# Performance work log

Measured on AMD Instinct MI355X. Metric: run time of the kernel, lower is better.

Reference implementation:

```python
import jax, jax.numpy as jnp
import numpy as np

NEG_INF = -1e30
LRELU_SLOPE = 0.2

B, E, IN_DIM, OUT_DIM = 64, 512, 1024, 256


def setup_inputs() -> dict:
    key = jax.random.key(0)
    ks = jax.random.split(key, 6)
    input_state = jax.random.normal(ks[0], (B, E, IN_DIM), dtype=jnp.float32)
    adj = jnp.ones((B, E, E), dtype=jnp.float32)  # only used via ones_like in the original
    node_mask = jax.random.randint(ks[1], (B, E, 1), 0, 2, dtype=jnp.int32)
    W_w = jax.random.normal(ks[2], (OUT_DIM, IN_DIM), dtype=jnp.float32) * (1.0 / np.sqrt(IN_DIM))
    W_b = jax.random.normal(ks[3], (OUT_DIM,), dtype=jnp.float32) * 0.02
    a_w = jax.random.normal(ks[4], (1, 2 * OUT_DIM), dtype=jnp.float32) * (1.0 / np.sqrt(2 * OUT_DIM))
    a_b = jax.random.normal(ks[5], (1,), dtype=jnp.float32) * 0.02
    return {"input_state": input_state, "adj": adj, "node_mask": node_mask,
            "W_w": W_w, "W_b": W_b, "a_w": a_w, "a_b": a_b}


def reference(input_state, adj, node_mask, W_w, W_b, a_w, a_b):
    # h = W(input_state); dropout is identity in eval mode (gnn_drop=0)
    h = jnp.einsum('bei,oi->beo', input_state, W_w) + W_b  # b,E,d
    d = h.shape[-1]
    # a([h_i ; h_j]) decomposes exactly: a_w[:, :d] @ h_i + a_w[:, d:] @ h_j + a_b
    a1, a2 = a_w[:, :d], a_w[:, d:]
    s1 = jnp.einsum('beo,xo->bex', h, a1)  # b,E,1 -> score contribution of source node i
    s2 = jnp.einsum('beo,xo->bex', h, a2)  # b,E,1 -> contribution of target node j
    scores = s1 + jnp.swapaxes(s2, 1, 2) + a_b  # b,E,E, scores[n,i,j] = a([h_i;h_j])
    scores = jnp.where(scores >= 0, scores, LRELU_SLOPE * scores)  # LeakyReLU(0.2)
    # fully-connected adjacency gated by node mask: mask_i * mask_j
    m = node_mask.astype(scores.dtype)  # b,E,1
    pair_mask = m * jnp.swapaxes(m, 1, 2)  # b,E,E
    scores = jnp.where(pair_mask > 0, scores, NEG_INF)
    coefs = jax.nn.softmax(scores, axis=-1)  # b,E,E
    h = h * m  # zero out masked nodes before aggregation
    return jnp.einsum('bij,bjo->bio', coefs, h)
```

## Files before the change

kernel.cpp:

```cpp
#include <hip/hip_runtime.h>
#include <hip/hip_fp16.h>
#include <math.h>

#define NEG_INF_F (-1e30f)
#define LRELU 0.2f

constexpr int Bb = 64, Ee = 512, IND = 1024, OUTD = 256;
constexpr int Mrows = Bb * Ee;

typedef __attribute__((ext_vector_type(8))) _Float16 half8;
typedef __attribute__((ext_vector_type(4))) _Float16 half4;
typedef __attribute__((ext_vector_type(4))) float floatx4;

#define AS1 __attribute__((address_space(1)))
#define AS3 __attribute__((address_space(3)))

__global__ __launch_bounds__(256) void wconv_kernel(
    const float* __restrict__ W, _Float16* __restrict__ Whf)
{
    const int i = (blockIdx.x * 256 + threadIdx.x) * 4;
    const float4 w = *reinterpret_cast<const float4*>(&W[i]);
    half4 hh;
    hh[0] = (_Float16)w.x; hh[1] = (_Float16)w.y;
    hh[2] = (_Float16)w.z; hh[3] = (_Float16)w.w;
    *reinterpret_cast<half4*>(&Whf[i]) = hh;
}

__global__ __launch_bounds__(256) void gemm_h_f16(
    const float* __restrict__ X, const _Float16* __restrict__ Whf,
    const float* __restrict__ Wb, const float* __restrict__ aw,
    const int* __restrict__ mask,
    _Float16* __restrict__ HmTh, _Float16* __restrict__ HmTl,
    float* __restrict__ s1, float* __restrict__ s2)
{
    __shared__ char lds_raw[81920];
    _Float16* As = (_Float16*)lds_raw;
    _Float16* Bs = (_Float16*)(lds_raw + 16384);
    float*    s1p  = (float*)lds_raw;
    float*    s2p  = (float*)(lds_raw + 1024);
    float*    mkfs = (float*)(lds_raw + 2048);
    _Float16* Th   = (_Float16*)(lds_raw + 16384);
    _Float16* Tl   = (_Float16*)(lds_raw + 49152);

    const int t  = threadIdx.x;
    const int w  = t >> 6;
    const int l  = t & 63;
    const int ln = l & 15;
    const int lg = l >> 4;
    const int m0 = blockIdx.x * 64;

    const int mA = t >> 3, pp = t & 7;
    const int aswz = pp ^ (mA & 7);
    const float* __restrict__ xbase = X + (size_t)m0 * IND;

    const int bn_sub = l >> 3;
    const int bkg = (l & 7) ^ (bn_sub & 7);

    floatx4 acc[4][4];
    #pragma unroll
    for (int i = 0; i < 4; ++i)
        #pragma unroll
        for (int j = 0; j < 4; ++j)
            acc[i][j] = (floatx4)0.f;

    auto loadA = [&](int k0, float4 xr[2][2]) {
        #pragma unroll
        for (int i = 0; i < 2; ++i) {
            const float* p = xbase + (size_t)(mA + 32 * i) * IND + k0 + pp * 8;
            xr[i][0] = *reinterpret_cast<const float4*>(p);
            xr[i][1] = *reinterpret_cast<const float4*>(p + 4);
        }
    };
    auto writeA = [&](int buf, float4 xr[2][2]) {
        #pragma unroll
        for (int i = 0; i < 2; ++i) {
            half8 h;
            h[0] = (_Float16)xr[i][0].x; h[1] = (_Float16)xr[i][0].y;
            h[2] = (_Float16)xr[i][0].z; h[3] = (_Float16)xr[i][0].w;
            h[4] = (_Float16)xr[i][1].x; h[5] = (_Float16)xr[i][1].y;
            h[6] = (_Float16)xr[i][1].z; h[7] = (_Float16)xr[i][1].w;
            *reinterpret_cast<half8*>(As + buf * 4096 + (mA + 32 * i) * 64 + aswz * 8) = h;
        }
    };
    auto stageB = [&](int buf, int k0) {
        #pragma unroll
        for (int j = 0; j < 8; ++j) {
            const int n = w * 64 + j * 8 + bn_sub;
            __builtin_amdgcn_global_load_lds(
                (const AS1 unsigned int*)(Whf + (size_t)n * IND + k0 + bkg * 8),
                (AS3 unsigned int*)(Bs + buf * 16384 + w * 4096 + j * 512),
                16, 0, 0);
        }
    };

    {
        float4 xr[2][2];
        loadA(0, xr);
        stageB(0, 0);
        writeA(0, xr);
    }
    __syncthreads();

    #pragma unroll 2
    for (int step = 0; step < 16; ++step) {
        const int buf = step & 1;
        float4 xn[2][2];
        if (step < 15) {
            loadA((step + 1) * 64, xn);
            stageB(buf ^ 1, (step + 1) * 64);
        }

        half8 af[2][4], bf[2][4];
        #pragma unroll
        for (int kk = 0; kk < 2; ++kk) {
            #pragma unroll
            for (int mr = 0; mr < 4; ++mr) {
                const int row = mr * 16 + ln;
                const int ch = (kk * 4 + lg) ^ (ln & 7);
                af[kk][mr] = *reinterpret_cast<const half8*>(As + buf * 4096 + row * 64 + ch * 8);
            }
            #pragma unroll
            for (int nr = 0; nr < 4; ++nr) {
                const int n = w * 64 + nr * 16 + ln;
                const int ch = (kk * 4 + lg) ^ (ln & 7);
                bf[kk][nr] = *reinterpret_cast<const half8*>(Bs + buf * 16384 + n * 64 + ch * 8);
            }
        }
        #pragma unroll
        for (int kk = 0; kk < 2; ++kk)
            #pragma unroll
            for (int mr = 0; mr < 4; ++mr)
                #pragma unroll
                for (int nr = 0; nr < 4; ++nr)
                    acc[mr][nr] = __builtin_amdgcn_mfma_f32_16x16x32_f16(
                        af[kk][mr], bf[kk][nr], acc[mr][nr], 0, 0, 0);

        if (step < 15) writeA(buf ^ 1, xn);
        __syncthreads();
    }

    if (t < 64) mkfs[t] = (float)mask[m0 + t];
    __syncthreads();

    float bias[4], a1c[4], a2c[4];
    #pragma unroll
    for (int nr = 0; nr < 4; ++nr) {
        const int n = w * 64 + nr * 16 + ln;
        bias[nr] = Wb[n];
        a1c[nr]  = aw[n];
        a2c[nr]  = aw[OUTD + n];
    }
    float sv1[4][4], sv2[4][4];
    #pragma unroll
    for (int i = 0; i < 4; ++i)
        #pragma unroll
        for (int r = 0; r < 4; ++r) { sv1[i][r] = 0.f; sv2[i][r] = 0.f; }

    #pragma unroll
    for (int mr = 0; mr < 4; ++mr)
        #pragma unroll
        for (int nr = 0; nr < 4; ++nr) {
            const int n = w * 64 + nr * 16 + ln;
            half4 hh, hl;
            #pragma unroll
            for (int rr = 0; rr < 4; ++rr) {
                const float hb = acc[mr][nr][rr] + bias[nr];
                sv1[mr][rr] += hb * a1c[nr];
                sv2[mr][rr] += hb * a2c[nr];
                const float hm = hb * mkfs[mr * 16 + lg * 4 + rr];
                const _Float16 hhi = (_Float16)hm;
                hh[rr] = hhi;
                hl[rr] = (_Float16)(hm - (float)hhi);
            }
            const int idx = n * 64 + ((mr * 16 + lg * 4) ^ ((n & 7) << 3));
            *reinterpret_cast<half4*>(Th + idx) = hh;
            *reinterpret_cast<half4*>(Tl + idx) = hl;
        }

    #pragma unroll
    for (int mr = 0; mr < 4; ++mr)
        #pragma unroll
        for (int rr = 0; rr < 4; ++rr) {
            float v1 = sv1[mr][rr], v2 = sv2[mr][rr];
            #pragma unroll
            for (int off = 1; off < 16; off <<= 1) {
                v1 += __shfl_xor(v1, off, 64);
                v2 += __shfl_xor(v2, off, 64);
            }
            if (ln == 0) {
                s1p[w * 64 + mr * 16 + lg * 4 + rr] = v1;
                s2p[w * 64 + mr * 16 + lg * 4 + rr] = v2;
            }
        }
    __syncthreads();

    if (t < 64) {
        s1[m0 + t] = s1p[t] + s1p[64 + t] + s1p[128 + t] + s1p[192 + t];
        s2[m0 + t] = s2p[t] + s2p[64 + t] + s2p[128 + t] + s2p[192 + t];
    }

    const int bIdx = m0 >> 9;
    const int e0   = m0 & 511;
    #pragma unroll
    for (int r4 = 0; r4 < 16; ++r4) {
        const int o = w * 64 + r4 * 4 + lg;
        const int src = o * 64 + ((ln * 4) ^ ((o & 7) << 3));
        const half4 vh = *reinterpret_cast<const half4*>(Th + src);
        const half4 vl = *reinterpret_cast<const half4*>(Tl + src);
        const size_t goff = ((size_t)(bIdx * OUTD + o) << 9) + e0 + ln * 4;
        *reinterpret_cast<half4*>(&HmTh[goff]) = vh;
        *reinterpret_cast<half4*>(&HmTl[goff]) = vl;
    }
}

__global__ __launch_bounds__(256, 2) void attn_mfma(
    const _Float16* __restrict__ HmTh, const _Float16* __restrict__ HmTl,
    const float* __restrict__ s1, const float* __restrict__ s2,
    const int* __restrict__ mask, const float* __restrict__ ab_ptr,
    float* __restrict__ Out)
{
    __shared__ float s2v[Ee];
    __shared__ float mkv[Ee];
    __shared__ float rowc[64];
    __shared__ float rmax[64];
    __shared__ int   rvv[64];
    __shared__ _Float16 Pl[2][64][32];
    __shared__ float Zp[64][4];
    __shared__ float zr[64];
    __shared__ float wmax[4];

    const int bid = blockIdx.x;
    const int b  = bid & 63;
    const int i0 = (bid >> 6) * 64;
    const int t  = threadIdx.x;
    const int w  = t >> 6, l = t & 63, ln = l & 15, lg = l >> 4;
    const float ab = ab_ptr[0];

    float lmax = -INFINITY;
    #pragma unroll
    for (int q = 0; q < 2; ++q) {
        const int j = t + q * 256;
        const float sv = s2[b * Ee + j];
        const float mv = (float)mask[b * Ee + j];
        s2v[j] = sv; mkv[j] = mv;
        if (mv > 0.f) lmax = fmaxf(lmax, sv);
    }
    #pragma unroll
    for (int off = 32; off; off >>= 1) lmax = fmaxf(lmax, __shfl_xor(lmax, off, 64));
    if (l == 0) wmax[w] = lmax;
    __syncthreads();
    const float s2max = fmaxf(fmaxf(wmax[0], wmax[1]), fmaxf(wmax[2], wmax[3]));
    const int anyvalid = (s2max > -1e37f) ? 1 : 0;
    if (t < 64) {
        const float c = s1[b * Ee + i0 + t] + ab;
        rowc[t] = c;
        const int mi = mask[b * Ee + i0 + t];
        rvv[t] = (mi != 0) & anyvalid;
        const float rm = c + s2max;
        rmax[t] = (rm >= 0.f) ? rm : LRELU * rm;
    }
    __syncthreads();

    const int pi = t >> 2;
    const int pj = (t & 3) * 8;
    const float prc = rowc[pi];
    const float prm = rmax[pi];
    const int   prv = rvv[pi];
    float zacc = 0.f;

    const size_t obase = (size_t)b * OUTD * Ee;
    const int o0 = w * 64;

    floatx4 acc[4][4];
    #pragma unroll
    for (int i = 0; i < 4; ++i)
        #pragma unroll
        for (int j = 0; j < 4; ++j)
            acc[i][j] = (floatx4)0.f;

    for (int ks = 0; ks < 16; ++ks) {
        const int k0  = ks * 32;
        const int buf = ks & 1;

        half8 ph;
        #pragma unroll
        for (int kk = 0; kk < 8; ++kk) {
            const int j = k0 + pj + kk;
            float pv;
            if (prv) {
                float sc = prc + s2v[j];
                sc = (sc >= 0.f) ? sc : LRELU * sc;
                pv = (mkv[j] > 0.f) ? __expf(sc - prm) : 0.f;
            } else {
                pv = 1.f;
            }
            const _Float16 hq = (_Float16)pv;
            ph[kk] = hq;
            zacc += (float)hq;
        }
        *reinterpret_cast<half8*>(&Pl[buf][pi][pj]) = ph;

        half8 bh[4], bl[4];
        #pragma unroll
        for (int ot = 0; ot < 4; ++ot) {
            const size_t ro = obase + (size_t)(o0 + ot * 16 + ln) * Ee + k0 + lg * 8;
            bh[ot] = *reinterpret_cast<const half8*>(&HmTh[ro]);
            bl[ot] = *reinterpret_cast<const half8*>(&HmTl[ro]);
        }
        __syncthreads();

        half8 af[4];
        #pragma unroll
        for (int mr = 0; mr < 4; ++mr)
            af[mr] = *reinterpret_cast<const half8*>(&Pl[buf][mr * 16 + ln][lg * 8]);
        #pragma unroll
        for (int mr = 0; mr < 4; ++mr)
            #pragma unroll
            for (int ot = 0; ot < 4; ++ot) {
                acc[mr][ot] = __builtin_amdgcn_mfma_f32_16x16x32_f16(
                    af[mr], bh[ot], acc[mr][ot], 0, 0, 0);
                acc[mr][ot] = __builtin_amdgcn_mfma_f32_16x16x32_f16(
                    af[mr], bl[ot], acc[mr][ot], 0, 0, 0);
            }
    }

    Zp[pi][t & 3] = zacc;
    __syncthreads();
    if (t < 64) {
        const float z = Zp[t][0] + Zp[t][1] + Zp[t][2] + Zp[t][3];
        zr[t] = 1.f / z;
    }
    __syncthreads();

    float* __restrict__ Ob = Out + ((size_t)b * Ee + i0) * OUTD;
    #pragma unroll
    for (int mr = 0; mr < 4; ++mr)
        #pragma unroll
        for (int rr = 0; rr < 4; ++rr) {
            const int i = mr * 16 + lg * 4 + rr;
            const float rzi = zr[i];
            #pragma unroll
            for (int ot = 0; ot < 4; ++ot)
                Ob[(size_t)i * OUTD + o0 + ot * 16 + ln] = acc[mr][ot][rr] * rzi;
        }
}

extern "C" void kernel_launch(void* const* d_in, const int* in_sizes, int n_in,
                              void* d_out, int out_size, void* d_ws, size_t ws_size,
                              hipStream_t stream) {
    const float* X    = (const float*)d_in[0];
    const int*   mask = (const int*)d_in[2];
    const float* Ww   = (const float*)d_in[3];
    const float* Wb   = (const float*)d_in[4];
    const float* aw   = (const float*)d_in[5];
    const float* ab   = (const float*)d_in[6];
    float* out = (float*)d_out;

    _Float16* HmTh = (_Float16*)d_ws;
    _Float16* HmTl = HmTh + (size_t)Bb * OUTD * Ee;
    float* s1 = (float*)(HmTl + (size_t)Bb * OUTD * Ee);
    float* s2 = s1 + Mrows;
    _Float16* Whf = (_Float16*)(s2 + Mrows);

    wconv_kernel<<<OUTD * IND / (256 * 4), 256, 0, stream>>>(Ww, Whf);
    gemm_h_f16<<<Mrows / 64, 256, 0, stream>>>(X, Whf, Wb, aw, mask,
                                               HmTh, HmTl, s1, s2);
    attn_mfma<<<Bb * (Ee / 64), 256, 0, stream>>>(HmTh, HmTl, s1, s2, mask, ab, out);
}
```

Baseline: 83.25 us.

## Enlarge projection GEMM tile to 128 rows with triple-buffered weight staging

The projection GEMM now computes 128-row tiles with 512 threads, arranged as 8 waves in a 2x4 grid. Each weight tile is therefore reused across twice as many rows, and there are half as many blocks. Weights are staged through a three-deep LDS ring, and X rows are double-buffered in registers. Explicit waitcnt, raw barriers and MFMA priority hints replace `__syncthreads`. Node masking moves from the per-element multiply into the final transposed write-out. The LDS footprint grows to about 133 KB per block, which limits residency to one block per CU and makes the hand-written wait counts fragile.

```diff
diff --git a/kernel.cpp b/kernel.cpp
--- a/kernel.cpp
+++ b/kernel.cpp
@@ -26,35 +26,33 @@
     *reinterpret_cast<half4*>(&Whf[i]) = hh;
 }
 
-__global__ __launch_bounds__(256) void gemm_h_f16(
+__global__ __launch_bounds__(512, 2) void gemm_h_f16(
     const float* __restrict__ X, const _Float16* __restrict__ Whf,
     const float* __restrict__ Wb, const float* __restrict__ aw,
     const int* __restrict__ mask,
     _Float16* __restrict__ HmTh, _Float16* __restrict__ HmTl,
     float* __restrict__ s1, float* __restrict__ s2)
 {
-    __shared__ char lds_raw[81920];
+    __shared__ char lds_raw[135680];
     _Float16* As = (_Float16*)lds_raw;
-    _Float16* Bs = (_Float16*)(lds_raw + 16384);
-    float*    s1p  = (float*)lds_raw;
-    float*    s2p  = (float*)(lds_raw + 1024);
-    float*    mkfs = (float*)(lds_raw + 2048);
-    _Float16* Th   = (_Float16*)(lds_raw + 16384);
-    _Float16* Tl   = (_Float16*)(lds_raw + 49152);
-
-    const int t  = threadIdx.x;
-    const int w  = t >> 6;
-    const int l  = t & 63;
-    const int ln = l & 15;
-    const int lg = l >> 4;
-    const int m0 = blockIdx.x * 64;
-
-    const int mA = t >> 3, pp = t & 7;
-    const int aswz = pp ^ (mA & 7);
-    const float* __restrict__ xbase = X + (size_t)m0 * IND;
-
-    const int bn_sub = l >> 3;
-    const int bkg = (l & 7) ^ (bn_sub & 7);
+    _Float16* Bs = (_Float16*)(lds_raw + 32768);
+    _Float16* Th = (_Float16*)lds_raw;
+    _Float16* Tl = (_Float16*)(lds_raw + 65536);
+    float* s1p  = (float*)(lds_raw + 131072);
+    float* s2p  = (float*)(lds_raw + 133120);
+    float* mkfs = (float*)(lds_raw + 135168);
+
+    const int tid = threadIdx.x;
+    const int w  = tid >> 6, l = tid & 63, ln = l & 15, lg = l >> 4;
+    const int wr = w >> 2, wc = w & 3;
+    const int m0 = blockIdx.x * 128;
+
+    const int arow = tid >> 2, ak = (tid & 3) * 16;
+    const float* __restrict__ xp = X + (size_t)(m0 + arow) * IND + ak;
+
+    const int brow_base = w * 32;
+    const int bsub = l >> 3;
+    const int bch  = (l & 7) ^ bsub;
 
     floatx4 acc[4][4];
     #pragma unroll
@@ -63,89 +61,111 @@
         for (int j = 0; j < 4; ++j)
             acc[i][j] = (floatx4)0.f;
 
-    auto loadA = [&](int k0, float4 xr[2][2]) {
-        #pragma unroll
-        for (int i = 0; i < 2; ++i) {
-            const float* p = xbase + (size_t)(mA + 32 * i) * IND + k0 + pp * 8;
-            xr[i][0] = *reinterpret_cast<const float4*>(p);
-            xr[i][1] = *reinterpret_cast<const float4*>(p + 4);
+    int bB0 = 0, bB1 = 1, bB2 = 2;
+
+    auto stageB = [&](int kc, int bufB) {
+        #pragma unroll
+        for (int j = 0; j < 4; ++j) {
+            const size_t src = (size_t)(brow_base + j * 8 + bsub) * IND + kc * 64 + bch * 8;
+            __builtin_amdgcn_global_load_lds(
+                (const AS1 unsigned int*)(Whf + src),
+                (AS3 unsigned int*)(Bs + bufB * 16384 + (brow_base + j * 8) * 64),
+                16, 0, 0);
         }
     };
-    auto writeA = [&](int buf, float4 xr[2][2]) {
-        #pragma unroll
-        for (int i = 0; i < 2; ++i) {
-            half8 h;
-            h[0] = (_Float16)xr[i][0].x; h[1] = (_Float16)xr[i][0].y;
-            h[2] = (_Float16)xr[i][0].z; h[3] = (_Float16)xr[i][0].w;
-            h[4] = (_Float16)xr[i][1].x; h[5] = (_Float16)xr[i][1].y;
-            h[6] = (_Float16)xr[i][1].z; h[7] = (_Float16)xr[i][1].w;
-            *reinterpret_cast<half8*>(As + buf * 4096 + (mA + 32 * i) * 64 + aswz * 8) = h;
-        }
+    auto writeA = [&](int abuf, const float4& r0, const float4& r1,
+                      const float4& r2, const float4& r3) {
+        half8 h0, h1;
+        h0[0] = (_Float16)r0.x; h0[1] = (_Float16)r0.y;
+        h0[2] = (_Float16)r0.z; h0[3] = (_Float16)r0.w;
+        h0[4] = (_Float16)r1.x; h0[5] = (_Float16)r1.y;
+        h0[6] = (_Float16)r1.z; h0[7] = (_Float16)r1.w;
+        h1[0] = (_Float16)r2.x; h1[1] = (_Float16)r2.y;
+        h1[2] = (_Float16)r2.z; h1[3] = (_Float16)r2.w;
+        h1[4] = (_Float16)r3.x; h1[5] = (_Float16)r3.y;
+        h1[6] = (_Float16)r3.z; h1[7] = (_Float16)r3.w;
+        const int c0 = (tid & 3) * 2;
+        *reinterpret_cast<half8*>(As + abuf * 8192 + arow * 64 + ((c0    ) ^ (arow & 7)) * 8) = h0;
+        *reinterpret_cast<half8*>(As + abuf * 8192 + arow * 64 + ((c0 + 1) ^ (arow & 7)) * 8) = h1;
     };
-    auto stageB = [&](int buf, int k0) {
-        #pragma unroll
-        for (int j = 0; j < 8; ++j) {
-            const int n = w * 64 + j * 8 + bn_sub;
-            __builtin_amdgcn_global_load_lds(
-                (const AS1 unsigned int*)(Whf + (size_t)n * IND + k0 + bkg * 8),
-                (AS3 unsigned int*)(Bs + buf * 16384 + w * 4096 + j * 512),
-                16, 0, 0);
-        }
-    };
+
+    float4 xa0, xa1, xa2, xa3, xb0, xb1, xb2, xb3;
 
     {
-        float4 xr[2][2];
-        loadA(0, xr);
+        const float4 p0 = *reinterpret_cast<const float4*>(xp + 0);
+        const float4 p1 = *reinterpret_cast<const float4*>(xp + 4);
+        const float4 p2 = *reinterpret_cast<const float4*>(xp + 8);
+        const float4 p3 = *reinterpret_cast<const float4*>(xp + 12);
+        xb0 = *reinterpret_cast<const float4*>(xp + 64);
+        xb1 = *reinterpret_cast<const float4*>(xp + 68);
+        xb2 = *reinterpret_cast<const float4*>(xp + 72);
+        xb3 = *reinterpret_cast<const float4*>(xp + 76);
         stageB(0, 0);
-        writeA(0, xr);
-    }
-    __syncthreads();
-
-    #pragma unroll 2
-    for (int step = 0; step < 16; ++step) {
-        const int buf = step & 1;
-        float4 xn[2][2];
-        if (step < 15) {
-            loadA((step + 1) * 64, xn);
-            stageB(buf ^ 1, (step + 1) * 64);
-        }
-
-        half8 af[2][4], bf[2][4];
+        stageB(1, 1);
+        writeA(0, p0, p1, p2, p3);
+        asm volatile("s_waitcnt vmcnt(4) lgkmcnt(0)" ::: "memory");
+        __builtin_amdgcn_sched_barrier(0);
+        __builtin_amdgcn_s_barrier();
+        __builtin_amdgcn_sched_barrier(0);
+    }
+
+    auto body = [&](int t,
+                    float4& L0, float4& L1, float4& L2, float4& L3,
+                    const float4& C0, const float4& C1,
+                    const float4& C2, const float4& C3) {
+        if (t < 14) {
+            const float* xq = xp + (t + 2) * 64;
+            L0 = *reinterpret_cast<const float4*>(xq + 0);
+            L1 = *reinterpret_cast<const float4*>(xq + 4);
+            L2 = *reinterpret_cast<const float4*>(xq + 8);
+            L3 = *reinterpret_cast<const float4*>(xq + 12);
+            stageB(t + 2, bB2);
+        }
+        __builtin_amdgcn_sched_barrier(0);
+
+        const int abuf = t & 1;
         #pragma unroll
         for (int kk = 0; kk < 2; ++kk) {
-            #pragma unroll
-            for (int mr = 0; mr < 4; ++mr) {
-                const int row = mr * 16 + ln;
-                const int ch = (kk * 4 + lg) ^ (ln & 7);
-                af[kk][mr] = *reinterpret_cast<const half8*>(As + buf * 4096 + row * 64 + ch * 8);
-            }
-            #pragma unroll
-            for (int nr = 0; nr < 4; ++nr) {
-                const int n = w * 64 + nr * 16 + ln;
-                const int ch = (kk * 4 + lg) ^ (ln & 7);
-                bf[kk][nr] = *reinterpret_cast<const half8*>(Bs + buf * 16384 + n * 64 + ch * 8);
-            }
-        }
-        #pragma unroll
-        for (int kk = 0; kk < 2; ++kk)
+            half8 af[4], bf[4];
+            #pragma unroll
+            for (int mr = 0; mr < 4; ++mr)
+                af[mr] = *reinterpret_cast<const half8*>(
+                    As + abuf * 8192 + (wr * 64 + mr * 16 + ln) * 64 + (((kk * 4 + lg) ^ (ln & 7)) * 8));
+            #pragma unroll
+            for (int nr = 0; nr < 4; ++nr)
+                bf[nr] = *reinterpret_cast<const half8*>(
+                    Bs + bB0 * 16384 + (wc * 64 + nr * 16 + ln) * 64 + (((kk * 4 + lg) ^ (ln & 7)) * 8));
+            __builtin_amdgcn_s_setprio(1);
             #pragma unroll
             for (int mr = 0; mr < 4; ++mr)
                 #pragma unroll
                 for (int nr = 0; nr < 4; ++nr)
                     acc[mr][nr] = __builtin_amdgcn_mfma_f32_16x16x32_f16(
-                        af[kk][mr], bf[kk][nr], acc[mr][nr], 0, 0, 0);
-
-        if (step < 15) writeA(buf ^ 1, xn);
-        __syncthreads();
-    }
-
-    if (t < 64) mkfs[t] = (float)mask[m0 + t];
-    __syncthreads();
+                        af[mr], bf[nr], acc[mr][nr], 0, 0, 0);
+            __builtin_amdgcn_s_setprio(0);
+        }
+
+        if (t < 15) writeA((t + 1) & 1, C0, C1, C2, C3);
+        if (t < 14) asm volatile("s_waitcnt vmcnt(8) lgkmcnt(0)" ::: "memory");
+        else        asm volatile("s_waitcnt vmcnt(0) lgkmcnt(0)" ::: "memory");
+        __builtin_amdgcn_sched_barrier(0);
+        __builtin_amdgcn_s_barrier();
+        __builtin_amdgcn_sched_barrier(0);
+        const int tmp = bB0; bB0 = bB1; bB1 = bB2; bB2 = tmp;
+    };
+
+    for (int p = 0; p < 8; ++p) {
+        body(2 * p,     xa0, xa1, xa2, xa3, xb0, xb1, xb2, xb3);
+        body(2 * p + 1, xb0, xb1, xb2, xb3, xa0, xa1, xa2, xa3);
+    }
+
+    __syncthreads();
+    if (tid < 128) mkfs[tid] = (float)mask[m0 + tid];
 
     float bias[4], a1c[4], a2c[4];
     #pragma unroll
     for (int nr = 0; nr < 4; ++nr) {
-        const int n = w * 64 + nr * 16 + ln;
+        const int n = wc * 64 + nr * 16 + ln;
         bias[nr] = Wb[n];
         a1c[nr]  = aw[n];
         a2c[nr]  = aw[OUTD + n];
@@ -160,19 +180,19 @@
     for (int mr = 0; mr < 4; ++mr)
         #pragma unroll
         for (int nr = 0; nr < 4; ++nr) {
-            const int n = w * 64 + nr * 16 + ln;
+            const int o = wc * 64 + nr * 16 + ln;
             half4 hh, hl;
             #pragma unroll
             for (int rr = 0; rr < 4; ++rr) {
                 const float hb = acc[mr][nr][rr] + bias[nr];
                 sv1[mr][rr] += hb * a1c[nr];
                 sv2[mr][rr] += hb * a2c[nr];
-                const float hm = hb * mkfs[mr * 16 + lg * 4 + rr];
-                const _Float16 hhi = (_Float16)hm;
+                const _Float16 hhi = (_Float16)hb;
                 hh[rr] = hhi;
-                hl[rr] = (_Float16)(hm - (float)hhi);
-            }
-            const int idx = n * 64 + ((mr * 16 + lg * 4) ^ ((n & 7) << 3));
+                hl[rr] = (_Float16)(hb - (float)hhi);
+            }
+            const int ebase = wr * 64 + mr * 16 + lg * 4;
+            const int idx = o * 128 + (ebase ^ ((o & 7) << 3));
             *reinterpret_cast<half4*>(Th + idx) = hh;
             *reinterpret_cast<half4*>(Tl + idx) = hl;
         }
@@ -188,26 +208,34 @@
                 v2 += __shfl_xor(v2, off, 64);
             }
             if (ln == 0) {
-                s1p[w * 64 + mr * 16 + lg * 4 + rr] = v1;
-                s2p[w * 64 + mr * 16 + lg * 4 + rr] = v2;
-            }
-        }
-    __syncthreads();
-
-    if (t < 64) {
-        s1[m0 + t] = s1p[t] + s1p[64 + t] + s1p[128 + t] + s1p[192 + t];
-        s2[m0 + t] = s2p[t] + s2p[64 + t] + s2p[128 + t] + s2p[192 + t];
+                const int e = wr * 64 + mr * 16 + lg * 4 + rr;
+                s1p[wc * 128 + e] = v1;
+                s2p[wc * 128 + e] = v2;
+            }
+        }
+    __syncthreads();
+
+    if (tid < 128) {
+        s1[m0 + tid] = s1p[tid] + s1p[128 + tid] + s1p[256 + tid] + s1p[384 + tid];
+        s2[m0 + tid] = s2p[tid] + s2p[128 + tid] + s2p[256 + tid] + s2p[384 + tid];
     }
 
     const int bIdx = m0 >> 9;
     const int e0   = m0 & 511;
-    #pragma unroll
-    for (int r4 = 0; r4 < 16; ++r4) {
-        const int o = w * 64 + r4 * 4 + lg;
-        const int src = o * 64 + ((ln * 4) ^ ((o & 7) << 3));
-        const half4 vh = *reinterpret_cast<const half4*>(Th + src);
-        const half4 vl = *reinterpret_cast<const half4*>(Tl + src);
-        const size_t goff = ((size_t)(bIdx * OUTD + o) << 9) + e0 + ln * 4;
+    const int eo4  = (tid & 31) * 4;
+    const float q0 = mkfs[eo4 + 0], q1 = mkfs[eo4 + 1];
+    const float q2 = mkfs[eo4 + 2], q3 = mkfs[eo4 + 3];
+    #pragma unroll
+    for (int it = 0; it < 16; ++it) {
+        const int o = it * 16 + (tid >> 5);
+        const int src = o * 128 + (eo4 ^ ((o & 7) << 3));
+        half4 vh = *reinterpret_cast<const half4*>(Th + src);
+        half4 vl = *reinterpret_cast<const half4*>(Tl + src);
+        if (!(q0 > 0.f)) { vh[0] = (_Float16)0.f; vl[0] = (_Float16)0.f; }
+        if (!(q1 > 0.f)) { vh[1] = (_Float16)0.f; vl[1] = (_Float16)0.f; }
+        if (!(q2 > 0.f)) { vh[2] = (_Float16)0.f; vl[2] = (_Float16)0.f; }
+        if (!(q3 > 0.f)) { vh[3] = (_Float16)0.f; vl[3] = (_Float16)0.f; }
+        const size_t goff = ((size_t)(bIdx * OUTD + o) << 9) + e0 + eo4;
         *reinterpret_cast<half4*>(&HmTh[goff]) = vh;
         *reinterpret_cast<half4*>(&HmTl[goff]) = vl;
     }
@@ -363,7 +391,7 @@
     _Float16* Whf = (_Float16*)(s2 + Mrows);
 
     wconv_kernel<<<OUTD * IND / (256 * 4), 256, 0, stream>>>(Ww, Whf);
-    gemm_h_f16<<<Mrows / 64, 256, 0, stream>>>(X, Whf, Wb, aw, mask,
-                                               HmTh, HmTl, s1, s2);
+    gemm_h_f16<<<Mrows / 128, 512, 0, stream>>>(X, Whf, Wb, aw, mask,
+                                                HmTh, HmTl, s1, s2);
     attn_mfma<<<Bb * (Ee / 64), 256, 0, stream>>>(HmTh, HmTl, s1, s2, mask, ab, out);
 }
```

Measured after the change: 89.85 us. +7.9%, slower.
